# Optimization experiments

Measured on AMD Instinct MI355X. Metric: run time of the kernel, lower is better.

## Reference

```python
import jax, jax.numpy as jnp
import numpy as np
from jax import lax

WINDOW_SIZE = 11
SIGMA = 1.5
MAX_VAL = 1.0
C1 = (MAX_VAL * 0.01) ** 2
C2 = (MAX_VAL * 0.03) ** 2


def _make_window(channel: int, k: int = WINDOW_SIZE, sigma: float = SIGMA) -> np.ndarray:
    x = np.arange(k, dtype=np.float64)
    g = np.exp(-((x - k // 2) ** 2) / (2.0 * sigma ** 2))
    g = (g / g.sum()).astype(np.float32)
    # rank-1 separable 3D window, built as dense [C,1,k,k,k] kernel (OIDHW, groups=C)
    w3 = g[:, None, None] * g[None, :, None] * g[None, None, :]
    return np.broadcast_to(w3, (channel, 1, k, k, k)).copy()


def _dwconv3d(x, kernel, pad):
    # depthwise 3D conv, SAME padding for odd kernel
    return lax.conv_general_dilated(
        x, kernel, window_strides=(1, 1, 1), padding=[(pad, pad)] * 3,
        dimension_numbers=("NCDHW", "OIDHW", "NCDHW"),
        feature_group_count=kernel.shape[0])


def setup_inputs() -> dict:
    key = jax.random.key(0)
    k1, k2 = jax.random.split(key)
    shape = (2, 4, 64, 160, 160)  # [B, C, D, H, W]
    img1 = jax.random.uniform(k1, shape, dtype=jnp.float32)
    img2 = jax.random.uniform(k2, shape, dtype=jnp.float32)
    return {"img1": img1, "img2": img2}


def reference(img1, img2):
    channel = img1.shape[1]
    window = jnp.asarray(_make_window(channel))
    pad = WINDOW_SIZE // 2
    # mask = ones_like(img1) in the original -> identity multiply, omitted
    mu1 = _dwconv3d(img1, window, pad)
    mu2 = _dwconv3d(img2, window, pad)
    mu1_sq = mu1 * mu1
    mu2_sq = mu2 * mu2
    mu1_mu2 = mu1 * mu2
    sigma1_sq = _dwconv3d(img1 * img1, window, pad) - mu1_sq
    sigma2_sq = _dwconv3d(img2 * img2, window, pad) - mu2_sq
    sigma12 = _dwconv3d(img1 * img2, window, pad) - mu1_mu2
    ssim_map = ((2.0 * mu1_mu2 + C1) * (2.0 * sigma12 + C2)) / (
        (mu1_sq + mu2_sq + C1) * (sigma1_sq + sigma2_sq + C2))
    ssim = jnp.mean(ssim_map, axis=(0, 2, 3, 4))  # per-channel SSIM, shape [C]
    return 1.0 - ssim
```

## Files before the change

### kernel.cpp

```cpp
#include <hip/hip_runtime.h>
#include <math.h>

typedef float v2f __attribute__((ext_vector_type(2)));

namespace {

constexpr int C_DIM = 4;
constexpr int D_DIM = 64;
constexpr int H_DIM = 160;
constexpr int W_DIM = 160;

constexpr int TH = 16;
constexpr int TW = 16;
constexpr int HALO = 5;
constexpr int EH = 26;
constexpr int EW = 26;
constexpr int XST = 27;
constexpr int MST = 17;
constexpr int NPIX = EH * EW;

constexpr int TILES_W = 10;
constexpr int TPC = 100;
constexpr int NBLOCKS = 2 * C_DIM * TPC;

constexpr float C1f = 1e-4f;
constexpr float C2f = 9e-4f;
constexpr float INV_N = 1.0f / (2.0f * 64.0f * 160.0f * 160.0f);

struct GW { float g[11]; };

}

__global__ void finalize_kernel(const float* __restrict__ partial,
                                float* __restrict__ out) {
    const int tid = threadIdx.x;
    const int c = tid >> 6;
    const int lane = tid & 63;
    float s = 0.0f;
#pragma unroll
    for (int b = 0; b < 2; ++b)
        for (int i = lane; i < TPC; i += 64)
            s += partial[b * (C_DIM * TPC) + c * TPC + i];
#pragma unroll
    for (int off = 32; off > 0; off >>= 1) s += __shfl_down(s, off, 64);
    if (lane == 0 && c < C_DIM) out[c] = 1.0f - s * INV_N;
}

__global__ __launch_bounds__(256, 4) void ssim3d_kernel(
    const float* __restrict__ img1, const float* __restrict__ img2,
    float* __restrict__ partial, GW gwp) {

    const int bid = blockIdx.x;
    const int tile = bid % TPC;
    const int c = (bid / TPC) % C_DIM;
    const int b = bid / (TPC * C_DIM);
    const int h0 = (tile / TILES_W) * TH;
    const int w0 = (tile % TILES_W) * TW;

    const long planeHW = (long)H_DIM * W_DIM;
    const long volbase = (long)(b * C_DIM + c) * D_DIM * planeHW;
    const long org = volbase + (long)(h0 - HALO) * W_DIM + (w0 - HALO);
    const float* __restrict__ p1 = img1 + org;
    const float* __restrict__ p2 = img2 + org;

    const bool interior = (h0 >= HALO) && (h0 + TH + HALO <= H_DIM) &&
                          (w0 >= HALO) && (w0 + TW + HALO <= W_DIM);

    __shared__ v2f    xy[2][EH][XST];
    __shared__ float4 mid[2][EH][MST];
    __shared__ float  rbuf[4];

    const int tid = threadIdx.x;

    int hh_[3], ww_[3], off_[3];
    bool live_[3], ok_[3];
#pragma unroll
    for (int k = 0; k < 3; ++k) {
        const int e = tid + k * 256;
        live_[k] = (e < NPIX);
        const int hh = e / EW;
        const int ww = e - hh * EW;
        hh_[k] = hh; ww_[k] = ww;
        off_[k] = hh * W_DIM + ww;
        const int gh = h0 - HALO + hh;
        const int gw = w0 - HALO + ww;
        ok_[k] = ((unsigned)gh < (unsigned)H_DIM) &&
                 ((unsigned)gw < (unsigned)W_DIM);
    }

    auto fetch_slice = [&](int s, v2f lv[3]) {
        const long sb = (long)s * planeHW;
#pragma unroll
        for (int k = 0; k < 3; ++k) {
            lv[k] = (v2f){0.0f, 0.0f};
            if (live_[k] && (interior || ok_[k])) {
                const long gi = sb + off_[k];
                lv[k].x = p1[gi];
                lv[k].y = p2[gi];
            }
        }
    };
    auto commit_slice = [&](int buf, const v2f lv[3]) {
#pragma unroll
        for (int k = 0; k < 3; ++k)
            if (live_[k]) xy[buf][hh_[k]][ww_[k]] = lv[k];
    };

    const bool wactive = (tid < 208);
    const int whh = tid % 26;
    const int wwg = (tid / 26) * 2;

    auto wconv = [&](int cur) {
        v2f a0 = {0.f, 0.f}, b0 = {0.f, 0.f};
        v2f a1 = {0.f, 0.f}, b1 = {0.f, 0.f};
#pragma unroll
        for (int t = 0; t < 12; ++t) {
            const v2f xv = xy[cur][whh][wwg + t];
            const v2f sq = xv * xv;
            v2f qp;
            qp.x = sq.x + sq.y;
            qp.y = xv.x * xv.y;
            if (t < 11) {
                const v2f g2 = {gwp.g[t], gwp.g[t]};
                a0 = __builtin_elementwise_fma(g2, xv, a0);
                b0 = __builtin_elementwise_fma(g2, qp, b0);
            }
            if (t >= 1) {
                const v2f g2 = {gwp.g[t - 1], gwp.g[t - 1]};
                a1 = __builtin_elementwise_fma(g2, xv, a1);
                b1 = __builtin_elementwise_fma(g2, qp, b1);
            }
        }
        mid[cur][whh][wwg]     = make_float4(a0.x, a0.y, b0.x, b0.y);
        mid[cur][whh][wwg + 1] = make_float4(a1.x, a1.y, b1.x, b1.y);
    };

    const int h_out = tid >> 4;
    const int w_out = tid & 15;
    auto hconv = [&](int cur, v2f& zxy, v2f& zqp) {
        zxy = (v2f){0.f, 0.f};
        zqp = (v2f){0.f, 0.f};
#pragma unroll
        for (int t = 0; t < 11; ++t) {
            const float4 m = mid[cur][h_out + t][w_out];
            const v2f g2 = {gwp.g[t], gwp.g[t]};
            const v2f ma = {m.x, m.y};
            const v2f mb = {m.z, m.w};
            zxy = __builtin_elementwise_fma(g2, ma, zxy);
            zqp = __builtin_elementwise_fma(g2, mb, zqp);
        }
    };

    float accum = 0.0f;
    auto ssim_add = [&](v2f mxy, v2f mqp) {
        const float m1 = mxy.x, m2 = mxy.y;
        const float q = mqp.x, pp = mqp.y;
        const float m1s = m1 * m1;
        const float m2s = m2 * m2;
        const float m12 = m1 * m2;
        const float spp = q - m1s - m2s;
        const float s12 = pp - m12;
        const float num = (2.0f * m12 + C1f) * (2.0f * s12 + C2f);
        const float den = (m1s + m2s + C1f) * (spp + C2f);
        accum = fmaf(num, __builtin_amdgcn_rcpf(den), accum);
    };

    v2f wxy[14], wqp[14];
#pragma unroll
    for (int i = 0; i < 14; ++i) {
        wxy[i] = (v2f){0.f, 0.f};
        wqp[i] = (v2f){0.f, 0.f};
    }

    {
        v2f lv[3];
        fetch_slice(0, lv);
        commit_slice(0, lv);
    }
    __syncthreads();

    for (int sb = 0; sb < D_DIM; sb += 4) {
#pragma unroll
        for (int u = 0; u < 4; ++u) {
            const int s = sb + u;
            v2f lv[3];
            const bool have_next = (s + 1 < D_DIM);
            if (have_next) fetch_slice(s + 1, lv);
            if (wactive) wconv(u & 1);
            if (have_next) commit_slice((u + 1) & 1, lv);
            __syncthreads();
            v2f zxy, zqp;
            hconv(u & 1, zxy, zqp);
            wxy[10 + u] = zxy;
            wqp[10 + u] = zqp;
            if (s >= HALO) {
                v2f mxy = {0.f, 0.f}, mqp = {0.f, 0.f};
#pragma unroll
                for (int t = 0; t < 11; ++t) {
                    const v2f g2 = {gwp.g[t], gwp.g[t]};
                    mxy = __builtin_elementwise_fma(g2, wxy[u + t], mxy);
                    mqp = __builtin_elementwise_fma(g2, wqp[u + t], mqp);
                }
                ssim_add(mxy, mqp);
            }
        }
#pragma unroll
        for (int k = 0; k < 10; ++k) {
            wxy[k] = wxy[k + 4];
            wqp[k] = wqp[k + 4];
        }
    }

#pragma unroll
    for (int i = 10; i < 14; ++i) {
        wxy[i] = (v2f){0.f, 0.f};
        wqp[i] = (v2f){0.f, 0.f};
    }
#pragma unroll
    for (int u2 = 0; u2 < 5; ++u2) {
        v2f mxy = {0.f, 0.f}, mqp = {0.f, 0.f};
#pragma unroll
        for (int t = 0; t < 11; ++t) {
            if (u2 + t <= 13) {
                const v2f g2 = {gwp.g[t], gwp.g[t]};
                mxy = __builtin_elementwise_fma(g2, wxy[u2 + t], mxy);
                mqp = __builtin_elementwise_fma(g2, wqp[u2 + t], mqp);
            }
        }
        ssim_add(mxy, mqp);
    }

#pragma unroll
    for (int off = 32; off > 0; off >>= 1) accum += __shfl_down(accum, off, 64);
    const int wave = tid >> 6;
    const int lane = tid & 63;
    if (lane == 0) rbuf[wave] = accum;
    __syncthreads();
    if (tid == 0) partial[bid] = rbuf[0] + rbuf[1] + rbuf[2] + rbuf[3];
}

extern "C" void kernel_launch(void* const* d_in, const int* in_sizes, int n_in,
                              void* d_out, int out_size, void* d_ws, size_t ws_size,
                              hipStream_t stream) {
    const float* img1 = (const float*)d_in[0];
    const float* img2 = (const float*)d_in[1];
    float* out = (float*)d_out;
    float* partial = (float*)d_ws;

    GW gw;
    {
        double gd[11];
        double ssum = 0.0;
        for (int i = 0; i < 11; ++i) {
            const double t = (double)(i - 5);
            gd[i] = exp(-(t * t) / 4.5);
            ssum += gd[i];
        }
        for (int i = 0; i < 11; ++i) gw.g[i] = (float)(gd[i] / ssum);
    }

    ssim3d_kernel<<<NBLOCKS, 256, 0, stream>>>(img1, img2, partial, gw);
    finalize_kernel<<<1, 256, 0, stream>>>(partial, out);
}
```

Measured before the change: 216.1 us.

## Enlarge spatial tile to 20x20 with register-blocked W and H passes

Grows each block's output tile from 16x16 to 20x20, which lowers the halo overhead per output pixel. The W-pass now produces four outputs per thread from a 14-tap window. The H-pass has 200 threads each produce two outputs and keep two depth rings in registers. Launch bounds drop to 2 blocks per SIMD to allow the larger register footprint, and only 512 blocks are launched. The cost is lower occupancy, idle threads in each pass (150 of 256 in W, 200 of 256 in H), and a grid that may not fill the GPU.

```diff
diff --git a/kernel.cpp b/kernel.cpp
--- a/kernel.cpp
+++ b/kernel.cpp
@@ -10,17 +10,17 @@
 constexpr int H_DIM = 160;
 constexpr int W_DIM = 160;
 
-constexpr int TH = 16;
-constexpr int TW = 16;
+constexpr int TH = 20;
+constexpr int TW = 20;
 constexpr int HALO = 5;
-constexpr int EH = 26;
-constexpr int EW = 26;
-constexpr int XST = 27;
-constexpr int MST = 17;
+constexpr int EH = 30;
+constexpr int EW = 30;
+constexpr int XST = 31;
+constexpr int MST = 21;
 constexpr int NPIX = EH * EW;
 
-constexpr int TILES_W = 10;
-constexpr int TPC = 100;
+constexpr int TILES_W = 8;
+constexpr int TPC = 64;
 constexpr int NBLOCKS = 2 * C_DIM * TPC;
 
 constexpr float C1f = 1e-4f;
@@ -36,17 +36,14 @@
     const int tid = threadIdx.x;
     const int c = tid >> 6;
     const int lane = tid & 63;
-    float s = 0.0f;
-#pragma unroll
-    for (int b = 0; b < 2; ++b)
-        for (int i = lane; i < TPC; i += 64)
-            s += partial[b * (C_DIM * TPC) + c * TPC + i];
+    float s = partial[c * TPC + lane] +
+              partial[C_DIM * TPC + c * TPC + lane];
 #pragma unroll
     for (int off = 32; off > 0; off >>= 1) s += __shfl_down(s, off, 64);
     if (lane == 0 && c < C_DIM) out[c] = 1.0f - s * INV_N;
 }
 
-__global__ __launch_bounds__(256, 4) void ssim3d_kernel(
+__global__ __launch_bounds__(256, 2) void ssim3d_kernel(
     const float* __restrict__ img1, const float* __restrict__ img2,
     float* __restrict__ partial, GW gwp) {
 
@@ -72,10 +69,10 @@
 
     const int tid = threadIdx.x;
 
-    int hh_[3], ww_[3], off_[3];
-    bool live_[3], ok_[3];
-#pragma unroll
-    for (int k = 0; k < 3; ++k) {
+    int hh_[4], ww_[4], off_[4];
+    bool live_[4], ok_[4];
+#pragma unroll
+    for (int k = 0; k < 4; ++k) {
         const int e = tid + k * 256;
         live_[k] = (e < NPIX);
         const int hh = e / EW;
@@ -88,10 +85,10 @@
                  ((unsigned)gw < (unsigned)W_DIM);
     }
 
-    auto fetch_slice = [&](int s, v2f lv[3]) {
+    auto fetch_slice = [&](int s, v2f lv[4]) {
         const long sb = (long)s * planeHW;
 #pragma unroll
-        for (int k = 0; k < 3; ++k) {
+        for (int k = 0; k < 4; ++k) {
             lv[k] = (v2f){0.0f, 0.0f};
             if (live_[k] && (interior || ok_[k])) {
                 const long gi = sb + off_[k];
@@ -100,56 +97,55 @@
             }
         }
     };
-    auto commit_slice = [&](int buf, const v2f lv[3]) {
-#pragma unroll
-        for (int k = 0; k < 3; ++k)
+    auto commit_slice = [&](int buf, const v2f lv[4]) {
+#pragma unroll
+        for (int k = 0; k < 4; ++k)
             if (live_[k]) xy[buf][hh_[k]][ww_[k]] = lv[k];
     };
 
-    const bool wactive = (tid < 208);
-    const int whh = tid % 26;
-    const int wwg = (tid / 26) * 2;
+    const bool wactive = (tid < 150);
+    const int whh = tid % 30;
+    const int wg  = (tid / 30) * 4;
 
     auto wconv = [&](int cur) {
-        v2f a0 = {0.f, 0.f}, b0 = {0.f, 0.f};
-        v2f a1 = {0.f, 0.f}, b1 = {0.f, 0.f};
-#pragma unroll
-        for (int t = 0; t < 12; ++t) {
-            const v2f xv = xy[cur][whh][wwg + t];
-            const v2f sq = xv * xv;
+        v2f a0 = {0.f,0.f}, a1 = {0.f,0.f}, a2 = {0.f,0.f}, a3 = {0.f,0.f};
+        v2f q0 = {0.f,0.f}, q1 = {0.f,0.f}, q2 = {0.f,0.f}, q3 = {0.f,0.f};
+#pragma unroll
+        for (int t = 0; t < 14; ++t) {
+            const v2f xv = xy[cur][whh][wg + t];
             v2f qp;
-            qp.x = sq.x + sq.y;
+            qp.x = fmaf(xv.x, xv.x, xv.y * xv.y);
             qp.y = xv.x * xv.y;
-            if (t < 11) {
+            if (t <= 10) {
                 const v2f g2 = {gwp.g[t], gwp.g[t]};
                 a0 = __builtin_elementwise_fma(g2, xv, a0);
-                b0 = __builtin_elementwise_fma(g2, qp, b0);
-            }
-            if (t >= 1) {
-                const v2f g2 = {gwp.g[t - 1], gwp.g[t - 1]};
+                q0 = __builtin_elementwise_fma(g2, qp, q0);
+            }
+            if (t >= 1 && t <= 11) {
+                const v2f g2 = {gwp.g[t-1], gwp.g[t-1]};
                 a1 = __builtin_elementwise_fma(g2, xv, a1);
-                b1 = __builtin_elementwise_fma(g2, qp, b1);
-            }
-        }
-        mid[cur][whh][wwg]     = make_float4(a0.x, a0.y, b0.x, b0.y);
-        mid[cur][whh][wwg + 1] = make_float4(a1.x, a1.y, b1.x, b1.y);
-    };
-
-    const int h_out = tid >> 4;
-    const int w_out = tid & 15;
-    auto hconv = [&](int cur, v2f& zxy, v2f& zqp) {
-        zxy = (v2f){0.f, 0.f};
-        zqp = (v2f){0.f, 0.f};
-#pragma unroll
-        for (int t = 0; t < 11; ++t) {
-            const float4 m = mid[cur][h_out + t][w_out];
-            const v2f g2 = {gwp.g[t], gwp.g[t]};
-            const v2f ma = {m.x, m.y};
-            const v2f mb = {m.z, m.w};
-            zxy = __builtin_elementwise_fma(g2, ma, zxy);
-            zqp = __builtin_elementwise_fma(g2, mb, zqp);
-        }
-    };
+                q1 = __builtin_elementwise_fma(g2, qp, q1);
+            }
+            if (t >= 2 && t <= 12) {
+                const v2f g2 = {gwp.g[t-2], gwp.g[t-2]};
+                a2 = __builtin_elementwise_fma(g2, xv, a2);
+                q2 = __builtin_elementwise_fma(g2, qp, q2);
+            }
+            if (t >= 3) {
+                const v2f g2 = {gwp.g[t-3], gwp.g[t-3]};
+                a3 = __builtin_elementwise_fma(g2, xv, a3);
+                q3 = __builtin_elementwise_fma(g2, qp, q3);
+            }
+        }
+        mid[cur][whh][wg]     = make_float4(a0.x, a0.y, q0.x, q0.y);
+        mid[cur][whh][wg + 1] = make_float4(a1.x, a1.y, q1.x, q1.y);
+        mid[cur][whh][wg + 2] = make_float4(a2.x, a2.y, q2.x, q2.y);
+        mid[cur][whh][wg + 3] = make_float4(a3.x, a3.y, q3.x, q3.y);
+    };
+
+    const bool hworker = (tid < 200);
+    const int hw = tid % 20;
+    const int hb = (tid / 20) * 2;
 
     float accum = 0.0f;
     auto ssim_add = [&](v2f mxy, v2f mqp) {
@@ -165,15 +161,15 @@
         accum = fmaf(num, __builtin_amdgcn_rcpf(den), accum);
     };
 
-    v2f wxy[14], wqp[14];
+    v2f w0xy[14], w0qp[14], w1xy[14], w1qp[14];
 #pragma unroll
     for (int i = 0; i < 14; ++i) {
-        wxy[i] = (v2f){0.f, 0.f};
-        wqp[i] = (v2f){0.f, 0.f};
+        w0xy[i] = (v2f){0.f, 0.f}; w0qp[i] = (v2f){0.f, 0.f};
+        w1xy[i] = (v2f){0.f, 0.f}; w1qp[i] = (v2f){0.f, 0.f};
     }
 
     {
-        v2f lv[3];
+        v2f lv[4];
         fetch_slice(0, lv);
         commit_slice(0, lv);
     }
@@ -183,51 +179,81 @@
 #pragma unroll
         for (int u = 0; u < 4; ++u) {
             const int s = sb + u;
-            v2f lv[3];
+            v2f lv[4];
             const bool have_next = (s + 1 < D_DIM);
             if (have_next) fetch_slice(s + 1, lv);
             if (wactive) wconv(u & 1);
             if (have_next) commit_slice((u + 1) & 1, lv);
             __syncthreads();
-            v2f zxy, zqp;
-            hconv(u & 1, zxy, zqp);
-            wxy[10 + u] = zxy;
-            wqp[10 + u] = zqp;
-            if (s >= HALO) {
-                v2f mxy = {0.f, 0.f}, mqp = {0.f, 0.f};
-#pragma unroll
-                for (int t = 0; t < 11; ++t) {
+            if (hworker) {
+                v2f z0x = {0.f,0.f}, z0q = {0.f,0.f};
+                v2f z1x = {0.f,0.f}, z1q = {0.f,0.f};
+#pragma unroll
+                for (int t = 0; t < 12; ++t) {
+                    const float4 m = mid[u & 1][hb + t][hw];
+                    const v2f ma = {m.x, m.y};
+                    const v2f mb = {m.z, m.w};
+                    if (t <= 10) {
+                        const v2f g2 = {gwp.g[t], gwp.g[t]};
+                        z0x = __builtin_elementwise_fma(g2, ma, z0x);
+                        z0q = __builtin_elementwise_fma(g2, mb, z0q);
+                    }
+                    if (t >= 1) {
+                        const v2f g2 = {gwp.g[t-1], gwp.g[t-1]};
+                        z1x = __builtin_elementwise_fma(g2, ma, z1x);
+                        z1q = __builtin_elementwise_fma(g2, mb, z1q);
+                    }
+                }
+                w0xy[10 + u] = z0x; w0qp[10 + u] = z0q;
+                w1xy[10 + u] = z1x; w1qp[10 + u] = z1q;
+                if (s >= HALO) {
+                    v2f mx0 = {0.f,0.f}, mq0 = {0.f,0.f};
+                    v2f mx1 = {0.f,0.f}, mq1 = {0.f,0.f};
+#pragma unroll
+                    for (int t = 0; t < 11; ++t) {
+                        const v2f g2 = {gwp.g[t], gwp.g[t]};
+                        mx0 = __builtin_elementwise_fma(g2, w0xy[u + t], mx0);
+                        mq0 = __builtin_elementwise_fma(g2, w0qp[u + t], mq0);
+                        mx1 = __builtin_elementwise_fma(g2, w1xy[u + t], mx1);
+                        mq1 = __builtin_elementwise_fma(g2, w1qp[u + t], mq1);
+                    }
+                    ssim_add(mx0, mq0);
+                    ssim_add(mx1, mq1);
+                }
+            }
+        }
+        if (hworker) {
+#pragma unroll
+            for (int k = 0; k < 10; ++k) {
+                w0xy[k] = w0xy[k + 4]; w0qp[k] = w0qp[k + 4];
+                w1xy[k] = w1xy[k + 4]; w1qp[k] = w1qp[k + 4];
+            }
+        }
+    }
+
+    if (hworker) {
+#pragma unroll
+        for (int i = 10; i < 14; ++i) {
+            w0xy[i] = (v2f){0.f, 0.f}; w0qp[i] = (v2f){0.f, 0.f};
+            w1xy[i] = (v2f){0.f, 0.f}; w1qp[i] = (v2f){0.f, 0.f};
+        }
+#pragma unroll
+        for (int u2 = 0; u2 < 5; ++u2) {
+            v2f mx0 = {0.f,0.f}, mq0 = {0.f,0.f};
+            v2f mx1 = {0.f,0.f}, mq1 = {0.f,0.f};
+#pragma unroll
+            for (int t = 0; t < 11; ++t) {
+                if (u2 + t <= 13) {
                     const v2f g2 = {gwp.g[t], gwp.g[t]};
-                    mxy = __builtin_elementwise_fma(g2, wxy[u + t], mxy);
-                    mqp = __builtin_elementwise_fma(g2, wqp[u + t], mqp);
+                    mx0 = __builtin_elementwise_fma(g2, w0xy[u2 + t], mx0);
+                    mq0 = __builtin_elementwise_fma(g2, w0qp[u2 + t], mq0);
+                    mx1 = __builtin_elementwise_fma(g2, w1xy[u2 + t], mx1);
+                    mq1 = __builtin_elementwise_fma(g2, w1qp[u2 + t], mq1);
                 }
-                ssim_add(mxy, mqp);
-            }
-        }
-#pragma unroll
-        for (int k = 0; k < 10; ++k) {
-            wxy[k] = wxy[k + 4];
-            wqp[k] = wqp[k + 4];
-        }
-    }
-
-#pragma unroll
-    for (int i = 10; i < 14; ++i) {
-        wxy[i] = (v2f){0.f, 0.f};
-        wqp[i] = (v2f){0.f, 0.f};
-    }
-#pragma unroll
-    for (int u2 = 0; u2 < 5; ++u2) {
-        v2f mxy = {0.f, 0.f}, mqp = {0.f, 0.f};
-#pragma unroll
-        for (int t = 0; t < 11; ++t) {
-            if (u2 + t <= 13) {
-                const v2f g2 = {gwp.g[t], gwp.g[t]};
-                mxy = __builtin_elementwise_fma(g2, wxy[u2 + t], mxy);
-                mqp = __builtin_elementwise_fma(g2, wqp[u2 + t], mqp);
-            }
-        }
-        ssim_add(mxy, mqp);
+            }
+            ssim_add(mx0, mq0);
+            ssim_add(mx1, mq1);
+        }
     }
 
 #pragma unroll
```

Result: faster. 208.0 us (-3.7%).
